# Optimization experiments

Measured on AMD Instinct MI355X. Metric: run time of the kernel, lower is better.

The kernel has to match this reference:

```python
import jax, jax.numpy as jnp
import numpy as np

N_NODES = 100000
N_EDGES = 3200000
N_GRAPHS = 1000
F_IN = 3
H = 64


def setup_inputs() -> dict:
    key = jax.random.key(0)
    ks = jax.random.split(key, 12)
    x = jax.random.normal(ks[0], (N_NODES, F_IN), dtype=jnp.float32)
    edge_index = jax.random.randint(ks[1], (2, N_EDGES), 0, N_NODES, dtype=jnp.int64)
    batch = jnp.sort(jax.random.randint(ks[2], (N_NODES,), 0, N_GRAPHS, dtype=jnp.int64))
    def lin(k, fan_in, fan_out):
        bound = 1.0 / np.sqrt(fan_in)
        return jax.random.uniform(k, (fan_in, fan_out), jnp.float32, -bound, bound)
    return {
        "x": x,
        "edge_index": edge_index,
        "batch": batch,
        "eps1": jax.random.uniform(ks[3], (), jnp.float32),
        "eps2": jax.random.uniform(ks[4], (), jnp.float32),
        "eps3": jax.random.uniform(ks[5], (), jnp.float32),
        "W1": lin(ks[6], F_IN, H), "b1": jnp.zeros((H,), jnp.float32),
        "W2": lin(ks[7], H, H),    "b2": jnp.zeros((H,), jnp.float32),
        "W3": lin(ks[8], H, H),    "b3": jnp.zeros((H,), jnp.float32),
        "Wf1": lin(ks[9], H, 10),  "bf1": jnp.zeros((10,), jnp.float32),
        "Wf2": lin(ks[10], 10, 1), "bf2": jnp.zeros((1,), jnp.float32),
    }


def gin_conv(x, src, dst, eps, W, b):
    # GIN: out = nn((1+eps)*x + sum_{j in N(i)} x_j)
    agg = jax.ops.segment_sum(x[src], dst, num_segments=N_NODES)
    h = (1.0 + eps) * x + agg
    return h @ W + b


def reference(x, edge_index, batch, eps1, eps2, eps3, W1, b1, W2, b2, W3, b3, Wf1, bf1, Wf2, bf2):
    src, dst = edge_index[0], edge_index[1]
    h = jax.nn.relu(gin_conv(x, src, dst, eps1, W1, b1))
    h = jax.nn.relu(gin_conv(h, src, dst, eps2, W2, b2))
    h = jax.nn.relu(gin_conv(h, src, dst, eps3, W3, b3))
    # global mean pool over graphs
    sums = jax.ops.segment_sum(h, batch, num_segments=N_GRAPHS)
    counts = jax.ops.segment_sum(jnp.ones((N_NODES, 1), h.dtype), batch, num_segments=N_GRAPHS)
    pooled = sums / jnp.maximum(counts, 1.0)
    out = jax.nn.relu(pooled @ Wf1 + bf1)
    return out @ Wf2 + bf2
```

## Files before the change

kernel.cpp:

```cpp
#include <hip/hip_runtime.h>

#define N_NODES  100000
#define N_EDGES  3200000
#define N_GRAPHS 1000
#define HDIM     64

#define BUCK_LOG 8
#define BUCK_SZ  256
#define NBUCK    ((N_NODES + BUCK_SZ - 1) / BUCK_SZ)
#define BIN_T    256
#define BIN_E    16
#define BIN_CHUNK (BIN_T * BIN_E)
#define CLUS_CAP 12288

typedef __attribute__((ext_vector_type(8))) short short8;
typedef __attribute__((ext_vector_type(4))) float f32x4;


__device__ inline unsigned short f2bf(float v) {
    unsigned int b; __builtin_memcpy(&b, &v, 4);
    return (unsigned short)((b + 0x7FFFu + ((b >> 16) & 1u)) >> 16);
}
__device__ inline float bf2f(unsigned short u) {
    return __uint_as_float(((unsigned int)u) << 16);
}
__device__ inline void sth(unsigned short* p, float v) { *p = f2bf(v); }
__device__ inline float bflo(unsigned int d) { return __uint_as_float(d << 16); }
__device__ inline float bfhi(unsigned int d) { return __uint_as_float(d & 0xFFFF0000u); }

__device__ inline int clampi(int v, int lo, int hi) {
    return v < lo ? lo : (v > hi ? hi : v);
}


__global__ void k_zero(int* __restrict__ p, int n) {
    int i = blockIdx.x * blockDim.x + threadIdx.x;
    if (i < n) p[i] = 0;
}


__global__ __launch_bounds__(BIN_T) void k_bcount(
        const int* __restrict__ ei, int* __restrict__ btot) {
    __shared__ int hist[NBUCK];
    for (int i = threadIdx.x; i < NBUCK; i += BIN_T) hist[i] = 0;
    __syncthreads();
    int e0 = blockIdx.x * BIN_CHUNK + threadIdx.x;
    #pragma unroll
    for (int k = 0; k < BIN_E; ++k) {
        int e = e0 + k * BIN_T;
        if (e < N_EDGES) {
            int d = clampi(ei[N_EDGES + e], 0, N_NODES - 1);
            atomicAdd(&hist[d >> BUCK_LOG], 1);
        }
    }
    __syncthreads();
    for (int i = threadIdx.x; i < NBUCK; i += BIN_T) {
        int c = hist[i];
        if (c) atomicAdd(&btot[i], c);
    }
}

__global__ void k_bscan(const int* __restrict__ btot, int* __restrict__ bbase,
                        int* __restrict__ gcur, int* __restrict__ off) {
    __shared__ int s[NBUCK + 1];
    int t = threadIdx.x;
    if (t < NBUCK) s[t] = btot[t];
    __syncthreads();
    if (t == 0) {
        int run = 0;
        for (int i = 0; i < NBUCK; ++i) { int x = s[i]; s[i] = run; run += x; }
        s[NBUCK] = run;
    }
    __syncthreads();
    if (t <= NBUCK) bbase[t] = s[t];
    if (t < NBUCK)  gcur[t] = s[t];
    if (t == 0)     off[N_NODES] = s[NBUCK];
}

__global__ __launch_bounds__(BIN_T) void k_bin(
        const int* __restrict__ ei, int* __restrict__ gcur,
        uint2* __restrict__ pairs) {
    __shared__ int hist[NBUCK];
    __shared__ int base[NBUCK];
    for (int i = threadIdx.x; i < NBUCK; i += BIN_T) hist[i] = 0;
    __syncthreads();
    int e0 = blockIdx.x * BIN_CHUNK + threadIdx.x;
    int d[BIN_E], s[BIN_E];
    #pragma unroll
    for (int k = 0; k < BIN_E; ++k) {
        int e = e0 + k * BIN_T;
        bool v = e < N_EDGES;
        d[k] = v ? clampi(ei[N_EDGES + e], 0, N_NODES - 1) : -1;
        s[k] = v ? clampi(ei[e], 0, N_NODES - 1) : 0;
        if (v) atomicAdd(&hist[d[k] >> BUCK_LOG], 1);
    }
    __syncthreads();
    for (int i = threadIdx.x; i < NBUCK; i += BIN_T) {
        int c = hist[i];
        base[i] = c ? atomicAdd(&gcur[i], c) : 0;
        hist[i] = 0;
    }
    __syncthreads();
    #pragma unroll
    for (int k = 0; k < BIN_E; ++k) {
        if (d[k] >= 0) {
            int b = d[k] >> BUCK_LOG;
            int r = atomicAdd(&hist[b], 1);
            uint2 p; p.x = (unsigned)d[k]; p.y = (unsigned)s[k];
            pairs[base[b] + r] = p;
        }
    }
}

__global__ __launch_bounds__(512) void k_cluster(
        const uint2* __restrict__ pairs, const int* __restrict__ bbase,
        int* __restrict__ off, int* __restrict__ adj) {
    __shared__ int ladj[CLUS_CAP];
    __shared__ int lcur[BUCK_SZ];
    __shared__ int lsc[BUCK_SZ];
    int b  = blockIdx.x;
    int lo = b * BUCK_SZ;
    int nn = N_NODES - lo; if (nn > BUCK_SZ) nn = BUCK_SZ;
    int e0 = bbase[b], e1 = bbase[b + 1];
    int cnt = e1 - e0;
    if (threadIdx.x < BUCK_SZ) lcur[threadIdx.x] = 0;
    __syncthreads();
    for (int i = threadIdx.x; i < cnt; i += 512) {
        uint2 p = pairs[e0 + i];
        atomicAdd(&lcur[p.x - lo], 1);
    }
    __syncthreads();
    int v = 0;
    if (threadIdx.x < BUCK_SZ) { v = lcur[threadIdx.x]; lsc[threadIdx.x] = v; }
    __syncthreads();
    #pragma unroll
    for (int d = 1; d < BUCK_SZ; d <<= 1) {
        int add = 0;
        if (threadIdx.x < BUCK_SZ && threadIdx.x >= d) add = lsc[threadIdx.x - d];
        __syncthreads();
        if (threadIdx.x < BUCK_SZ) lsc[threadIdx.x] += add;
        __syncthreads();
    }
    if (threadIdx.x < BUCK_SZ) {
        int exc = lsc[threadIdx.x] - v;
        if (threadIdx.x < nn) off[lo + threadIdx.x] = e0 + exc;
        lcur[threadIdx.x] = exc;
    }
    __syncthreads();
    if (cnt <= CLUS_CAP) {
        for (int i = threadIdx.x; i < cnt; i += 512) {
            uint2 p = pairs[e0 + i];
            int pos = atomicAdd(&lcur[p.x - lo], 1);
            ladj[pos] = (int)p.y;
        }
        __syncthreads();
        for (int i = threadIdx.x; i < cnt; i += 512) adj[e0 + i] = ladj[i];
    } else {
        for (int i = threadIdx.x; i < cnt; i += 512) {
            uint2 p = pairs[e0 + i];
            int pos = atomicAdd(&lcur[p.x - lo], 1);
            adj[e0 + pos] = (int)p.y;
        }
    }
}


__global__ __launch_bounds__(256) void k_layer1(
        const float* __restrict__ x, const int* __restrict__ off,
        const int* __restrict__ adj, const float* __restrict__ epsp,
        const float* __restrict__ W1, const float* __restrict__ b1,
        unsigned short* __restrict__ hout) {
    int wid  = (blockIdx.x * blockDim.x + threadIdx.x) >> 6;
    int lane = threadIdx.x & 63;
    if (wid >= N_NODES) return;
    int o0 = off[wid], o1 = off[wid + 1];
    float a0 = 0.f, a1 = 0.f, a2 = 0.f;
    for (int e = o0 + lane; e < o1; e += 64) {
        int s = adj[e];
        a0 += x[s * 3 + 0];
        a1 += x[s * 3 + 1];
        a2 += x[s * 3 + 2];
    }
    #pragma unroll
    for (int d = 32; d; d >>= 1) {
        a0 += __shfl_xor(a0, d);
        a1 += __shfl_xor(a1, d);
        a2 += __shfl_xor(a2, d);
    }
    float ep = 1.0f + epsp[0];
    float s0 = ep * x[wid * 3 + 0] + a0;
    float s1 = ep * x[wid * 3 + 1] + a1;
    float s2 = ep * x[wid * 3 + 2] + a2;
    float o = b1[lane] + s0 * W1[lane] + s1 * W1[64 + lane] + s2 * W1[128 + lane];
    sth(&hout[(size_t)wid * 64 + lane], fmaxf(o, 0.f));
}


__global__ __launch_bounds__(256) void k_gemm(
        const unsigned short* __restrict__ hin, const float* __restrict__ W,
        unsigned short* __restrict__ Y) {
    int lane = threadIdx.x & 63;
    int r = lane & 15;
    int g = lane >> 4;
    int wave   = blockIdx.x * (blockDim.x >> 6) + (threadIdx.x >> 6);
    int nwaves = gridDim.x * (blockDim.x >> 6);

    short8 bh[2][4], bl[2][4];
    #pragma unroll
    for (int s = 0; s < 2; ++s) {
        #pragma unroll
        for (int t = 0; t < 4; ++t) {
            short8 hv, lv;
            #pragma unroll
            for (int i = 0; i < 8; ++i) {
                int k = s * 32 + g * 8 + i;
                int n = t * 16 + r;
                float w = W[k * 64 + n];
                unsigned short wh = f2bf(w);
                float whf = bf2f(wh);
                hv[i] = (short)wh;
                lv[i] = (short)f2bf(w - whf);
            }
            bh[s][t] = hv; bl[s][t] = lv;
        }
    }

    const int NT = N_NODES / 16;
    for (int mt = wave; mt < NT; mt += nwaves) {
        const unsigned short* arow = hin + (size_t)(mt * 16 + r) * 64;
        short8 a0 = *(const short8*)(arow + g * 8);
        short8 a1 = *(const short8*)(arow + 32 + g * 8);
        #pragma unroll
        for (int t = 0; t < 4; ++t) {
            f32x4 acc = {0.f, 0.f, 0.f, 0.f};
            acc = __builtin_amdgcn_mfma_f32_16x16x32_bf16(a0, bh[0][t], acc, 0, 0, 0);
            acc = __builtin_amdgcn_mfma_f32_16x16x32_bf16(a0, bl[0][t], acc, 0, 0, 0);
            acc = __builtin_amdgcn_mfma_f32_16x16x32_bf16(a1, bh[1][t], acc, 0, 0, 0);
            acc = __builtin_amdgcn_mfma_f32_16x16x32_bf16(a1, bl[1][t], acc, 0, 0, 0);
            #pragma unroll
            for (int j = 0; j < 4; ++j) {
                sth(&Y[(size_t)(mt * 16 + g * 4 + j) * 64 + t * 16 + r], acc[j]);
            }
        }
    }
}


__device__ inline void gather_node(
        const uint2* __restrict__ h2, const int* __restrict__ off,
        const int* __restrict__ adj, int node, int sl, int g4,
        float& a0, float& a1, float& a2, float& a3) {
    int o0 = off[node], o1 = off[node + 1];
    int deg = o1 - o0;
    int nchunk = (deg + 15) >> 4;
    for (int c = 0; c < nchunk; ++c) {
        int pos = o0 + (c << 4) + sl;
        int posc = pos < o1 ? pos : (o1 - 1);
        int idxv = adj[posc];
        int rem = deg - (c << 4);
        #pragma unroll
        for (int half = 0; half < 2; ++half) {
            uint2 dd[8];
            #pragma unroll
            for (int i = 0; i < 8; ++i) {
                int k = half * 8 + i;
                int s = __shfl(idxv, (g4 << 4) + k);
                dd[i] = h2[(size_t)s * 16 + sl];
            }
            #pragma unroll
            for (int i = 0; i < 8; ++i) {
                int k = half * 8 + i;
                int ok = k < rem;
                unsigned int lo = ok ? dd[i].x : 0u;
                unsigned int hc = ok ? dd[i].y : 0u;
                a0 += bflo(lo); a1 += bfhi(lo);
                a2 += bflo(hc); a3 += bfhi(hc);
            }
            if (rem <= 8) break;
        }
    }
}

__global__ __launch_bounds__(1024) void k_gather(
        const unsigned short* __restrict__ Y, const int* __restrict__ off,
        const int* __restrict__ adj, const float* __restrict__ epsp,
        const float* __restrict__ b, unsigned short* __restrict__ hout) {
    int tid  = blockIdx.x * 1024 + threadIdx.x;
    int node = tid >> 4;
    if (node >= N_NODES) return;
    int sl = threadIdx.x & 15;
    int g4 = (threadIdx.x >> 4) & 3;
    const uint2* h2 = (const uint2*)Y;
    float a0 = 0.f, a1 = 0.f, a2 = 0.f, a3 = 0.f;
    gather_node(h2, off, adj, node, sl, g4, a0, a1, a2, a3);
    uint2 ds = h2[(size_t)node * 16 + sl];
    float ep = 1.0f + epsp[0];
    a0 = fmaxf(a0 + ep * bflo(ds.x) + b[4 * sl + 0], 0.f);
    a1 = fmaxf(a1 + ep * bfhi(ds.x) + b[4 * sl + 1], 0.f);
    a2 = fmaxf(a2 + ep * bflo(ds.y) + b[4 * sl + 2], 0.f);
    a3 = fmaxf(a3 + ep * bfhi(ds.y) + b[4 * sl + 3], 0.f);
    uint2 o;
    o.x = (unsigned int)f2bf(a0) | ((unsigned int)f2bf(a1) << 16);
    o.y = (unsigned int)f2bf(a2) | ((unsigned int)f2bf(a3) << 16);
    ((uint2*)hout)[(size_t)node * 16 + sl] = o;
}

__global__ __launch_bounds__(1024) void k_gather_pool(
        const unsigned short* __restrict__ Y, const int* __restrict__ off,
        const int* __restrict__ adj, const float* __restrict__ epsp,
        const float* __restrict__ b, const int* __restrict__ batch,
        float* __restrict__ pooled, int* __restrict__ cnt) {
    __shared__ float sacc[8 * 64];
    __shared__ int   scnt[8];
    for (int i = threadIdx.x; i < 8 * 64; i += 1024) sacc[i] = 0.f;
    if (threadIdx.x < 8) scnt[threadIdx.x] = 0;
    __syncthreads();

    int tid  = blockIdx.x * 1024 + threadIdx.x;
    int node = tid >> 4;
    int sl = threadIdx.x & 15;
    int g4 = (threadIdx.x >> 4) & 3;
    int g0 = clampi(batch[clampi(blockIdx.x << 6, 0, N_NODES - 1)], 0, N_GRAPHS - 1);

    if (node < N_NODES) {
        const uint2* h2 = (const uint2*)Y;
        float a0 = 0.f, a1 = 0.f, a2 = 0.f, a3 = 0.f;
        gather_node(h2, off, adj, node, sl, g4, a0, a1, a2, a3);
        uint2 ds = h2[(size_t)node * 16 + sl];
        float ep = 1.0f + epsp[0];
        a0 = fmaxf(a0 + ep * bflo(ds.x) + b[4 * sl + 0], 0.f);
        a1 = fmaxf(a1 + ep * bfhi(ds.x) + b[4 * sl + 1], 0.f);
        a2 = fmaxf(a2 + ep * bflo(ds.y) + b[4 * sl + 2], 0.f);
        a3 = fmaxf(a3 + ep * bfhi(ds.y) + b[4 * sl + 3], 0.f);
        int g  = clampi(batch[node], 0, N_GRAPHS - 1);
        int og = g - g0;
        if (og >= 0 && og < 8) {
            atomicAdd(&sacc[og * 64 + 4 * sl + 0], a0);
            atomicAdd(&sacc[og * 64 + 4 * sl + 1], a1);
            atomicAdd(&sacc[og * 64 + 4 * sl + 2], a2);
            atomicAdd(&sacc[og * 64 + 4 * sl + 3], a3);
            if (sl == 0) atomicAdd(&scnt[og], 1);
        } else {
            atomicAdd(&pooled[g * 64 + 4 * sl + 0], a0);
            atomicAdd(&pooled[g * 64 + 4 * sl + 1], a1);
            atomicAdd(&pooled[g * 64 + 4 * sl + 2], a2);
            atomicAdd(&pooled[g * 64 + 4 * sl + 3], a3);
            if (sl == 0) atomicAdd(&cnt[g], 1);
        }
    }
    __syncthreads();
    int w = threadIdx.x >> 6;
    int lane = threadIdx.x & 63;
    if (w < 8) {
        int c = scnt[w];
        if (c > 0) {
            atomicAdd(&pooled[(g0 + w) * 64 + lane], sacc[w * 64 + lane]);
            if (lane == 0) atomicAdd(&cnt[g0 + w], c);
        }
    }
}


__global__ __launch_bounds__(256) void k_head(
        const float* __restrict__ pooled, const int* __restrict__ cnt,
        const float* __restrict__ Wf1, const float* __restrict__ bf1,
        const float* __restrict__ Wf2, const float* __restrict__ bf2,
        float* __restrict__ out) {
    int g = blockIdx.x * blockDim.x + threadIdx.x;
    if (g >= N_GRAPHS) return;
    float inv = 1.0f / fmaxf((float)cnt[g], 1.0f);
    float p[64];
    #pragma unroll
    for (int k = 0; k < 64; ++k) p[k] = pooled[g * 64 + k] * inv;
    float o = bf2[0];
    #pragma unroll
    for (int j = 0; j < 10; ++j) {
        float s = bf1[j];
        #pragma unroll
        for (int k = 0; k < 64; ++k) s += p[k] * Wf1[k * 10 + j];
        o += fmaxf(s, 0.f) * Wf2[j];
    }
    out[g] = o;
}


extern "C" void kernel_launch(void* const* d_in, const int* in_sizes, int n_in,
                              void* d_out, int out_size, void* d_ws, size_t ws_size,
                              hipStream_t stream) {
    const float* x     = (const float*)d_in[0];
    const int*   ei    = (const int*)d_in[1];
    const int*   batch = (const int*)d_in[2];
    const float* eps1 = (const float*)d_in[3];
    const float* eps2 = (const float*)d_in[4];
    const float* eps3 = (const float*)d_in[5];
    const float* W1 = (const float*)d_in[6];
    const float* b1 = (const float*)d_in[7];
    const float* W2 = (const float*)d_in[8];
    const float* b2 = (const float*)d_in[9];
    const float* W3 = (const float*)d_in[10];
    const float* b3 = (const float*)d_in[11];
    const float* Wf1 = (const float*)d_in[12];
    const float* bf1 = (const float*)d_in[13];
    const float* Wf2 = (const float*)d_in[14];
    const float* bf2 = (const float*)d_in[15];
    float* out = (float*)d_out;

    const size_t H64 = (size_t)N_NODES * HDIM;

    char* base = (char*)d_ws;
    unsigned short* hA = (unsigned short*)base;
    unsigned short* hB = (unsigned short*)(base + H64 * 2);
    uint2* pairs = (uint2*)base;
    char* q = base + 2 * H64 * 2;
    float* pooled = (float*)q;            q += 64000ull * 4;
    int*   cnt    = (int*)q;              q += 1000ull * 4;
    int*   off    = (int*)q;              q += 100004ull * 4;
    int*   btot   = (int*)q;              q += 512ull * 4;
    int*   bbase  = (int*)q;              q += 512ull * 4;
    int*   gcur   = (int*)q;              q += 512ull * 4;
    int*   adj    = (int*)q;

    const int TB = 256;
    k_zero<<<(65000 + TB - 1) / TB, TB, 0, stream>>>((int*)pooled, 65000);
    k_zero<<<2, TB, 0, stream>>>(btot, NBUCK);

    const int BINB = (N_EDGES + BIN_CHUNK - 1) / BIN_CHUNK;
    k_bcount<<<BINB, BIN_T, 0, stream>>>(ei, btot);
    k_bscan<<<1, 512, 0, stream>>>(btot, bbase, gcur, off);
    k_bin<<<BINB, BIN_T, 0, stream>>>(ei, gcur, pairs);
    k_cluster<<<NBUCK, 512, 0, stream>>>(pairs, bbase, off, adj);

    const int L1_BLOCKS = (int)((H64 + TB - 1) / TB);
    const int GB = (N_NODES * 16 + 1023) / 1024;

    k_layer1<<<L1_BLOCKS, TB, 0, stream>>>(x, off, adj, eps1, W1, b1, hA);
    k_gemm<<<256, 256, 0, stream>>>(hA, W2, hB);
    k_gather<<<GB, 1024, 0, stream>>>(hB, off, adj, eps2, b2, hA);
    k_gemm<<<256, 256, 0, stream>>>(hA, W3, hB);
    k_gather_pool<<<GB, 1024, 0, stream>>>(hB, off, adj, eps3, b3, batch, pooled, cnt);

    k_head<<<(N_GRAPHS + TB - 1) / TB, TB, 0, stream>>>(pooled, cnt, Wf1, bf1, Wf2, bf2, out);
}
```

Before: 283.5 us.

## Vectorize edge binning loads, pack pairs to 32-bit, widen gather to 8 lanes/node

Edge binning kernels now have each thread read 16 contiguous edges through int4 vector loads instead of strided scalar loads. Binned pairs are packed into one 32-bit word holding the in-bucket dst offset and the src index, which halves the pair traffic between binning and clustering. The neighbor gather kernels use 8 lanes per node with 16-byte loads and 8 edges per chunk, in place of 16 lanes with 8-byte loads and 16-edge chunks. The packing assumes src indices fit in 24 bits, and with fewer lanes per node each lane does more serial work per neighbor.

```diff
diff --git a/kernel.cpp b/kernel.cpp
--- a/kernel.cpp
+++ b/kernel.cpp
@@ -15,6 +15,8 @@
 
 typedef __attribute__((ext_vector_type(8))) short short8;
 typedef __attribute__((ext_vector_type(4))) float f32x4;
+typedef __attribute__((ext_vector_type(4))) int   int4v;
+typedef __attribute__((ext_vector_type(4))) unsigned uint4v;
 
 
 __device__ inline unsigned short f2bf(float v) {
@@ -44,13 +46,25 @@
     __shared__ int hist[NBUCK];
     for (int i = threadIdx.x; i < NBUCK; i += BIN_T) hist[i] = 0;
     __syncthreads();
-    int e0 = blockIdx.x * BIN_CHUNK + threadIdx.x;
-    #pragma unroll
-    for (int k = 0; k < BIN_E; ++k) {
-        int e = e0 + k * BIN_T;
-        if (e < N_EDGES) {
-            int d = clampi(ei[N_EDGES + e], 0, N_NODES - 1);
-            atomicAdd(&hist[d >> BUCK_LOG], 1);
+    int e0 = blockIdx.x * BIN_CHUNK + threadIdx.x * BIN_E;
+    if (e0 + BIN_E <= N_EDGES) {
+        const int4v* d4 = (const int4v*)(ei + N_EDGES);
+        #pragma unroll
+        for (int q = 0; q < 4; ++q) {
+            int4v dv = d4[(e0 >> 2) + q];
+            #pragma unroll
+            for (int j = 0; j < 4; ++j) {
+                int d = clampi(dv[j], 0, N_NODES - 1);
+                atomicAdd(&hist[d >> BUCK_LOG], 1);
+            }
+        }
+    } else {
+        for (int k = 0; k < BIN_E; ++k) {
+            int e = e0 + k;
+            if (e < N_EDGES) {
+                int d = clampi(ei[N_EDGES + e], 0, N_NODES - 1);
+                atomicAdd(&hist[d >> BUCK_LOG], 1);
+            }
         }
     }
     __syncthreads();
@@ -79,20 +93,36 @@
 
 __global__ __launch_bounds__(BIN_T) void k_bin(
         const int* __restrict__ ei, int* __restrict__ gcur,
-        uint2* __restrict__ pairs) {
+        unsigned* __restrict__ pairs) {
     __shared__ int hist[NBUCK];
     __shared__ int base[NBUCK];
     for (int i = threadIdx.x; i < NBUCK; i += BIN_T) hist[i] = 0;
     __syncthreads();
-    int e0 = blockIdx.x * BIN_CHUNK + threadIdx.x;
+    int e0 = blockIdx.x * BIN_CHUNK + threadIdx.x * BIN_E;
     int d[BIN_E], s[BIN_E];
-    #pragma unroll
-    for (int k = 0; k < BIN_E; ++k) {
-        int e = e0 + k * BIN_T;
-        bool v = e < N_EDGES;
-        d[k] = v ? clampi(ei[N_EDGES + e], 0, N_NODES - 1) : -1;
-        s[k] = v ? clampi(ei[e], 0, N_NODES - 1) : 0;
-        if (v) atomicAdd(&hist[d[k] >> BUCK_LOG], 1);
+    if (e0 + BIN_E <= N_EDGES) {
+        const int4v* s4 = (const int4v*)ei;
+        const int4v* d4 = (const int4v*)(ei + N_EDGES);
+        #pragma unroll
+        for (int q = 0; q < 4; ++q) {
+            int4v dv = d4[(e0 >> 2) + q];
+            int4v sv = s4[(e0 >> 2) + q];
+            #pragma unroll
+            for (int j = 0; j < 4; ++j) {
+                d[q * 4 + j] = clampi(dv[j], 0, N_NODES - 1);
+                s[q * 4 + j] = clampi(sv[j], 0, N_NODES - 1);
+            }
+        }
+        #pragma unroll
+        for (int k = 0; k < BIN_E; ++k) atomicAdd(&hist[d[k] >> BUCK_LOG], 1);
+    } else {
+        for (int k = 0; k < BIN_E; ++k) {
+            int e = e0 + k;
+            bool v = e < N_EDGES;
+            d[k] = v ? clampi(ei[N_EDGES + e], 0, N_NODES - 1) : -1;
+            s[k] = v ? clampi(ei[e], 0, N_NODES - 1) : 0;
+            if (v) atomicAdd(&hist[d[k] >> BUCK_LOG], 1);
+        }
     }
     __syncthreads();
     for (int i = threadIdx.x; i < NBUCK; i += BIN_T) {
@@ -106,14 +136,13 @@
         if (d[k] >= 0) {
             int b = d[k] >> BUCK_LOG;
             int r = atomicAdd(&hist[b], 1);
-            uint2 p; p.x = (unsigned)d[k]; p.y = (unsigned)s[k];
-            pairs[base[b] + r] = p;
+            pairs[base[b] + r] = ((unsigned)(d[k] & (BUCK_SZ - 1)) << 24) | (unsigned)s[k];
         }
     }
 }
 
 __global__ __launch_bounds__(512) void k_cluster(
-        const uint2* __restrict__ pairs, const int* __restrict__ bbase,
+        const unsigned* __restrict__ pairs, const int* __restrict__ bbase,
         int* __restrict__ off, int* __restrict__ adj) {
     __shared__ int ladj[CLUS_CAP];
     __shared__ int lcur[BUCK_SZ];
@@ -126,8 +155,8 @@
     if (threadIdx.x < BUCK_SZ) lcur[threadIdx.x] = 0;
     __syncthreads();
     for (int i = threadIdx.x; i < cnt; i += 512) {
-        uint2 p = pairs[e0 + i];
-        atomicAdd(&lcur[p.x - lo], 1);
+        unsigned p = pairs[e0 + i];
+        atomicAdd(&lcur[p >> 24], 1);
     }
     __syncthreads();
     int v = 0;
@@ -149,17 +178,17 @@
     __syncthreads();
     if (cnt <= CLUS_CAP) {
         for (int i = threadIdx.x; i < cnt; i += 512) {
-            uint2 p = pairs[e0 + i];
-            int pos = atomicAdd(&lcur[p.x - lo], 1);
-            ladj[pos] = (int)p.y;
+            unsigned p = pairs[e0 + i];
+            int pos = atomicAdd(&lcur[p >> 24], 1);
+            ladj[pos] = (int)(p & 0xFFFFFFu);
         }
         __syncthreads();
         for (int i = threadIdx.x; i < cnt; i += 512) adj[e0 + i] = ladj[i];
     } else {
         for (int i = threadIdx.x; i < cnt; i += 512) {
-            uint2 p = pairs[e0 + i];
-            int pos = atomicAdd(&lcur[p.x - lo], 1);
-            adj[e0 + pos] = (int)p.y;
+            unsigned p = pairs[e0 + i];
+            int pos = atomicAdd(&lcur[p >> 24], 1);
+            adj[e0 + pos] = (int)(p & 0xFFFFFFu);
         }
     }
 }
@@ -246,37 +275,33 @@
 }
 
 
-__device__ inline void gather_node(
-        const uint2* __restrict__ h2, const int* __restrict__ off,
-        const int* __restrict__ adj, int node, int sl, int g4,
-        float& a0, float& a1, float& a2, float& a3) {
+__device__ inline void gather8(
+        const uint4v* __restrict__ h4, const int* __restrict__ off,
+        const int* __restrict__ adj, int node, int sl, int g8, float acc[8]) {
     int o0 = off[node], o1 = off[node + 1];
     int deg = o1 - o0;
-    int nchunk = (deg + 15) >> 4;
-    for (int c = 0; c < nchunk; ++c) {
-        int pos = o0 + (c << 4) + sl;
+    for (int base = 0; base < deg; base += 8) {
+        int pos = o0 + base + sl;
         int posc = pos < o1 ? pos : (o1 - 1);
         int idxv = adj[posc];
-        int rem = deg - (c << 4);
-        #pragma unroll
-        for (int half = 0; half < 2; ++half) {
-            uint2 dd[8];
-            #pragma unroll
-            for (int i = 0; i < 8; ++i) {
-                int k = half * 8 + i;
-                int s = __shfl(idxv, (g4 << 4) + k);
-                dd[i] = h2[(size_t)s * 16 + sl];
-            }
-            #pragma unroll
-            for (int i = 0; i < 8; ++i) {
-                int k = half * 8 + i;
-                int ok = k < rem;
-                unsigned int lo = ok ? dd[i].x : 0u;
-                unsigned int hc = ok ? dd[i].y : 0u;
-                a0 += bflo(lo); a1 += bfhi(lo);
-                a2 += bflo(hc); a3 += bfhi(hc);
-            }
-            if (rem <= 8) break;
+        int rem = deg - base;
+        uint4v dd[8];
+        #pragma unroll
+        for (int k = 0; k < 8; ++k) {
+            int s = __shfl(idxv, (g8 << 3) + k);
+            dd[k] = h4[(size_t)s * 8 + sl];
+        }
+        #pragma unroll
+        for (int k = 0; k < 8; ++k) {
+            bool ok = k < rem;
+            unsigned x0 = ok ? dd[k][0] : 0u;
+            unsigned x1 = ok ? dd[k][1] : 0u;
+            unsigned x2 = ok ? dd[k][2] : 0u;
+            unsigned x3 = ok ? dd[k][3] : 0u;
+            acc[0] += bflo(x0); acc[1] += bfhi(x0);
+            acc[2] += bflo(x1); acc[3] += bfhi(x1);
+            acc[4] += bflo(x2); acc[5] += bfhi(x2);
+            acc[6] += bflo(x3); acc[7] += bfhi(x3);
         }
     }
 }
@@ -286,23 +311,27 @@
         const int* __restrict__ adj, const float* __restrict__ epsp,
         const float* __restrict__ b, unsigned short* __restrict__ hout) {
     int tid  = blockIdx.x * 1024 + threadIdx.x;
-    int node = tid >> 4;
+    int node = tid >> 3;
     if (node >= N_NODES) return;
-    int sl = threadIdx.x & 15;
-    int g4 = (threadIdx.x >> 4) & 3;
-    const uint2* h2 = (const uint2*)Y;
-    float a0 = 0.f, a1 = 0.f, a2 = 0.f, a3 = 0.f;
-    gather_node(h2, off, adj, node, sl, g4, a0, a1, a2, a3);
-    uint2 ds = h2[(size_t)node * 16 + sl];
+    int sl = threadIdx.x & 7;
+    int g8 = (threadIdx.x >> 3) & 7;
+    const uint4v* h4 = (const uint4v*)Y;
+    float acc[8] = {0.f, 0.f, 0.f, 0.f, 0.f, 0.f, 0.f, 0.f};
+    gather8(h4, off, adj, node, sl, g8, acc);
+    uint4v ds = h4[(size_t)node * 8 + sl];
     float ep = 1.0f + epsp[0];
-    a0 = fmaxf(a0 + ep * bflo(ds.x) + b[4 * sl + 0], 0.f);
-    a1 = fmaxf(a1 + ep * bfhi(ds.x) + b[4 * sl + 1], 0.f);
-    a2 = fmaxf(a2 + ep * bflo(ds.y) + b[4 * sl + 2], 0.f);
-    a3 = fmaxf(a3 + ep * bfhi(ds.y) + b[4 * sl + 3], 0.f);
-    uint2 o;
-    o.x = (unsigned int)f2bf(a0) | ((unsigned int)f2bf(a1) << 16);
-    o.y = (unsigned int)f2bf(a2) | ((unsigned int)f2bf(a3) << 16);
-    ((uint2*)hout)[(size_t)node * 16 + sl] = o;
+    acc[0] += ep * bflo(ds[0]); acc[1] += ep * bfhi(ds[0]);
+    acc[2] += ep * bflo(ds[1]); acc[3] += ep * bfhi(ds[1]);
+    acc[4] += ep * bflo(ds[2]); acc[5] += ep * bfhi(ds[2]);
+    acc[6] += ep * bflo(ds[3]); acc[7] += ep * bfhi(ds[3]);
+    uint4v o;
+    #pragma unroll
+    for (int i = 0; i < 4; ++i) {
+        float lo = fmaxf(acc[2 * i]     + b[8 * sl + 2 * i],     0.f);
+        float hi = fmaxf(acc[2 * i + 1] + b[8 * sl + 2 * i + 1], 0.f);
+        o[i] = (unsigned)f2bf(lo) | ((unsigned)f2bf(hi) << 16);
+    }
+    ((uint4v*)hout)[(size_t)node * 8 + sl] = o;
 }
 
 __global__ __launch_bounds__(1024) void k_gather_pool(
@@ -317,34 +346,32 @@
     __syncthreads();
 
     int tid  = blockIdx.x * 1024 + threadIdx.x;
-    int node = tid >> 4;
-    int sl = threadIdx.x & 15;
-    int g4 = (threadIdx.x >> 4) & 3;
-    int g0 = clampi(batch[clampi(blockIdx.x << 6, 0, N_NODES - 1)], 0, N_GRAPHS - 1);
+    int node = tid >> 3;
+    int sl = threadIdx.x & 7;
+    int g8 = (threadIdx.x >> 3) & 7;
+    int g0 = clampi(batch[clampi(blockIdx.x << 7, 0, N_NODES - 1)], 0, N_GRAPHS - 1);
 
     if (node < N_NODES) {
-        const uint2* h2 = (const uint2*)Y;
-        float a0 = 0.f, a1 = 0.f, a2 = 0.f, a3 = 0.f;
-        gather_node(h2, off, adj, node, sl, g4, a0, a1, a2, a3);
-        uint2 ds = h2[(size_t)node * 16 + sl];
+        const uint4v* h4 = (const uint4v*)Y;
+        float acc[8] = {0.f, 0.f, 0.f, 0.f, 0.f, 0.f, 0.f, 0.f};
+        gather8(h4, off, adj, node, sl, g8, acc);
+        uint4v ds = h4[(size_t)node * 8 + sl];
         float ep = 1.0f + epsp[0];
-        a0 = fmaxf(a0 + ep * bflo(ds.x) + b[4 * sl + 0], 0.f);
-        a1 = fmaxf(a1 + ep * bfhi(ds.x) + b[4 * sl + 1], 0.f);
-        a2 = fmaxf(a2 + ep * bflo(ds.y) + b[4 * sl + 2], 0.f);
-        a3 = fmaxf(a3 + ep * bfhi(ds.y) + b[4 * sl + 3], 0.f);
+        acc[0] += ep * bflo(ds[0]); acc[1] += ep * bfhi(ds[0]);
+        acc[2] += ep * bflo(ds[1]); acc[3] += ep * bfhi(ds[1]);
+        acc[4] += ep * bflo(ds[2]); acc[5] += ep * bfhi(ds[2]);
+        acc[6] += ep * bflo(ds[3]); acc[7] += ep * bfhi(ds[3]);
         int g  = clampi(batch[node], 0, N_GRAPHS - 1);
         int og = g - g0;
         if (og >= 0 && og < 8) {
-            atomicAdd(&sacc[og * 64 + 4 * sl + 0], a0);
-            atomicAdd(&sacc[og * 64 + 4 * sl + 1], a1);
-            atomicAdd(&sacc[og * 64 + 4 * sl + 2], a2);
-            atomicAdd(&sacc[og * 64 + 4 * sl + 3], a3);
+            #pragma unroll
+            for (int i = 0; i < 8; ++i)
+                atomicAdd(&sacc[og * 64 + 8 * sl + i], fmaxf(acc[i] + b[8 * sl + i], 0.f));
             if (sl == 0) atomicAdd(&scnt[og], 1);
         } else {
-            atomicAdd(&pooled[g * 64 + 4 * sl + 0], a0);
-            atomicAdd(&pooled[g * 64 + 4 * sl + 1], a1);
-            atomicAdd(&pooled[g * 64 + 4 * sl + 2], a2);
-            atomicAdd(&pooled[g * 64 + 4 * sl + 3], a3);
+            #pragma unroll
+            for (int i = 0; i < 8; ++i)
+                atomicAdd(&pooled[g * 64 + 8 * sl + i], fmaxf(acc[i] + b[8 * sl + i], 0.f));
             if (sl == 0) atomicAdd(&cnt[g], 1);
         }
     }
@@ -410,7 +437,7 @@
     char* base = (char*)d_ws;
     unsigned short* hA = (unsigned short*)base;
     unsigned short* hB = (unsigned short*)(base + H64 * 2);
-    uint2* pairs = (uint2*)base;
+    unsigned* pairs = (unsigned*)base;
     char* q = base + 2 * H64 * 2;
     float* pooled = (float*)q;            q += 64000ull * 4;
     int*   cnt    = (int*)q;              q += 1000ull * 4;
@@ -431,7 +458,7 @@
     k_cluster<<<NBUCK, 512, 0, stream>>>(pairs, bbase, off, adj);
 
     const int L1_BLOCKS = (int)((H64 + TB - 1) / TB);
-    const int GB = (N_NODES * 16 + 1023) / 1024;
+    const int GB = (N_NODES * 8 + 1023) / 1024;
 
     k_layer1<<<L1_BLOCKS, TB, 0, stream>>>(x, off, adj, eps1, W1, b1, hA);
     k_gemm<<<256, 256, 0, stream>>>(hA, W2, hB);
```

After: 305.4 us. 7.7% more time.

## Vectorize edge loads in binning, pack pairs to 32-bit, shrink gather blocks

Applied to the files above, without the earlier changes.

The binning kernels now give each thread a contiguous run of 16 edges and load them with 128-bit vector reads instead of strided scalar reads. Each binned pair is packed into one 32-bit word: the bucket-local destination in the top 8 bits and the source in the low 24. This halves the pairs traffic written by k_bin and read twice by k_cluster. The gather kernels drop from 1024 to 512 threads per block, which should help scheduling and occupancy; the packing relies on node ids fitting in 24 bits.

```diff
diff --git a/kernel.cpp b/kernel.cpp
--- a/kernel.cpp
+++ b/kernel.cpp
@@ -15,6 +15,7 @@
 
 typedef __attribute__((ext_vector_type(8))) short short8;
 typedef __attribute__((ext_vector_type(4))) float f32x4;
+typedef __attribute__((ext_vector_type(4))) int   int4v;
 
 
 __device__ inline unsigned short f2bf(float v) {
@@ -44,13 +45,25 @@
     __shared__ int hist[NBUCK];
     for (int i = threadIdx.x; i < NBUCK; i += BIN_T) hist[i] = 0;
     __syncthreads();
-    int e0 = blockIdx.x * BIN_CHUNK + threadIdx.x;
-    #pragma unroll
-    for (int k = 0; k < BIN_E; ++k) {
-        int e = e0 + k * BIN_T;
-        if (e < N_EDGES) {
-            int d = clampi(ei[N_EDGES + e], 0, N_NODES - 1);
-            atomicAdd(&hist[d >> BUCK_LOG], 1);
+    int e0 = blockIdx.x * BIN_CHUNK + threadIdx.x * BIN_E;
+    if (e0 + BIN_E <= N_EDGES) {
+        const int4v* d4 = (const int4v*)(ei + N_EDGES);
+        #pragma unroll
+        for (int q = 0; q < 4; ++q) {
+            int4v dv = d4[(e0 >> 2) + q];
+            #pragma unroll
+            for (int j = 0; j < 4; ++j) {
+                int d = clampi(dv[j], 0, N_NODES - 1);
+                atomicAdd(&hist[d >> BUCK_LOG], 1);
+            }
+        }
+    } else {
+        for (int k = 0; k < BIN_E; ++k) {
+            int e = e0 + k;
+            if (e < N_EDGES) {
+                int d = clampi(ei[N_EDGES + e], 0, N_NODES - 1);
+                atomicAdd(&hist[d >> BUCK_LOG], 1);
+            }
         }
     }
     __syncthreads();
@@ -79,20 +92,36 @@
 
 __global__ __launch_bounds__(BIN_T) void k_bin(
         const int* __restrict__ ei, int* __restrict__ gcur,
-        uint2* __restrict__ pairs) {
+        unsigned* __restrict__ pairs) {
     __shared__ int hist[NBUCK];
     __shared__ int base[NBUCK];
     for (int i = threadIdx.x; i < NBUCK; i += BIN_T) hist[i] = 0;
     __syncthreads();
-    int e0 = blockIdx.x * BIN_CHUNK + threadIdx.x;
+    int e0 = blockIdx.x * BIN_CHUNK + threadIdx.x * BIN_E;
     int d[BIN_E], s[BIN_E];
-    #pragma unroll
-    for (int k = 0; k < BIN_E; ++k) {
-        int e = e0 + k * BIN_T;
-        bool v = e < N_EDGES;
-        d[k] = v ? clampi(ei[N_EDGES + e], 0, N_NODES - 1) : -1;
-        s[k] = v ? clampi(ei[e], 0, N_NODES - 1) : 0;
-        if (v) atomicAdd(&hist[d[k] >> BUCK_LOG], 1);
+    if (e0 + BIN_E <= N_EDGES) {
+        const int4v* s4 = (const int4v*)ei;
+        const int4v* d4 = (const int4v*)(ei + N_EDGES);
+        #pragma unroll
+        for (int q = 0; q < 4; ++q) {
+            int4v dv = d4[(e0 >> 2) + q];
+            int4v sv = s4[(e0 >> 2) + q];
+            #pragma unroll
+            for (int j = 0; j < 4; ++j) {
+                d[q * 4 + j] = clampi(dv[j], 0, N_NODES - 1);
+                s[q * 4 + j] = clampi(sv[j], 0, N_NODES - 1);
+            }
+        }
+        #pragma unroll
+        for (int k = 0; k < BIN_E; ++k) atomicAdd(&hist[d[k] >> BUCK_LOG], 1);
+    } else {
+        for (int k = 0; k < BIN_E; ++k) {
+            int e = e0 + k;
+            bool v = e < N_EDGES;
+            d[k] = v ? clampi(ei[N_EDGES + e], 0, N_NODES - 1) : -1;
+            s[k] = v ? clampi(ei[e], 0, N_NODES - 1) : 0;
+            if (v) atomicAdd(&hist[d[k] >> BUCK_LOG], 1);
+        }
     }
     __syncthreads();
     for (int i = threadIdx.x; i < NBUCK; i += BIN_T) {
@@ -106,14 +135,13 @@
         if (d[k] >= 0) {
             int b = d[k] >> BUCK_LOG;
             int r = atomicAdd(&hist[b], 1);
-            uint2 p; p.x = (unsigned)d[k]; p.y = (unsigned)s[k];
-            pairs[base[b] + r] = p;
+            pairs[base[b] + r] = ((unsigned)(d[k] & (BUCK_SZ - 1)) << 24) | (unsigned)s[k];
         }
     }
 }
 
 __global__ __launch_bounds__(512) void k_cluster(
-        const uint2* __restrict__ pairs, const int* __restrict__ bbase,
+        const unsigned* __restrict__ pairs, const int* __restrict__ bbase,
         int* __restrict__ off, int* __restrict__ adj) {
     __shared__ int ladj[CLUS_CAP];
     __shared__ int lcur[BUCK_SZ];
@@ -126,8 +154,8 @@
     if (threadIdx.x < BUCK_SZ) lcur[threadIdx.x] = 0;
     __syncthreads();
     for (int i = threadIdx.x; i < cnt; i += 512) {
-        uint2 p = pairs[e0 + i];
-        atomicAdd(&lcur[p.x - lo], 1);
+        unsigned p = pairs[e0 + i];
+        atomicAdd(&lcur[p >> 24], 1);
     }
     __syncthreads();
     int v = 0;
@@ -149,17 +177,17 @@
     __syncthreads();
     if (cnt <= CLUS_CAP) {
         for (int i = threadIdx.x; i < cnt; i += 512) {
-            uint2 p = pairs[e0 + i];
-            int pos = atomicAdd(&lcur[p.x - lo], 1);
-            ladj[pos] = (int)p.y;
+            unsigned p = pairs[e0 + i];
+            int pos = atomicAdd(&lcur[p >> 24], 1);
+            ladj[pos] = (int)(p & 0xFFFFFFu);
         }
         __syncthreads();
         for (int i = threadIdx.x; i < cnt; i += 512) adj[e0 + i] = ladj[i];
     } else {
         for (int i = threadIdx.x; i < cnt; i += 512) {
-            uint2 p = pairs[e0 + i];
-            int pos = atomicAdd(&lcur[p.x - lo], 1);
-            adj[e0 + pos] = (int)p.y;
+            unsigned p = pairs[e0 + i];
+            int pos = atomicAdd(&lcur[p >> 24], 1);
+            adj[e0 + pos] = (int)(p & 0xFFFFFFu);
         }
     }
 }
@@ -281,11 +309,11 @@
     }
 }
 
-__global__ __launch_bounds__(1024) void k_gather(
+__global__ __launch_bounds__(512) void k_gather(
         const unsigned short* __restrict__ Y, const int* __restrict__ off,
         const int* __restrict__ adj, const float* __restrict__ epsp,
         const float* __restrict__ b, unsigned short* __restrict__ hout) {
-    int tid  = blockIdx.x * 1024 + threadIdx.x;
+    int tid  = blockIdx.x * 512 + threadIdx.x;
     int node = tid >> 4;
     if (node >= N_NODES) return;
     int sl = threadIdx.x & 15;
@@ -305,22 +333,22 @@
     ((uint2*)hout)[(size_t)node * 16 + sl] = o;
 }
 
-__global__ __launch_bounds__(1024) void k_gather_pool(
+__global__ __launch_bounds__(512) void k_gather_pool(
         const unsigned short* __restrict__ Y, const int* __restrict__ off,
         const int* __restrict__ adj, const float* __restrict__ epsp,
         const float* __restrict__ b, const int* __restrict__ batch,
         float* __restrict__ pooled, int* __restrict__ cnt) {
     __shared__ float sacc[8 * 64];
     __shared__ int   scnt[8];
-    for (int i = threadIdx.x; i < 8 * 64; i += 1024) sacc[i] = 0.f;
+    for (int i = threadIdx.x; i < 8 * 64; i += 512) sacc[i] = 0.f;
     if (threadIdx.x < 8) scnt[threadIdx.x] = 0;
     __syncthreads();
 
-    int tid  = blockIdx.x * 1024 + threadIdx.x;
+    int tid  = blockIdx.x * 512 + threadIdx.x;
     int node = tid >> 4;
     int sl = threadIdx.x & 15;
     int g4 = (threadIdx.x >> 4) & 3;
-    int g0 = clampi(batch[clampi(blockIdx.x << 6, 0, N_NODES - 1)], 0, N_GRAPHS - 1);
+    int g0 = clampi(batch[clampi(blockIdx.x * 32, 0, N_NODES - 1)], 0, N_GRAPHS - 1);
 
     if (node < N_NODES) {
         const uint2* h2 = (const uint2*)Y;
@@ -410,7 +438,7 @@
     char* base = (char*)d_ws;
     unsigned short* hA = (unsigned short*)base;
     unsigned short* hB = (unsigned short*)(base + H64 * 2);
-    uint2* pairs = (uint2*)base;
+    unsigned* pairs = (unsigned*)base;
     char* q = base + 2 * H64 * 2;
     float* pooled = (float*)q;            q += 64000ull * 4;
     int*   cnt    = (int*)q;              q += 1000ull * 4;
@@ -431,13 +459,13 @@
     k_cluster<<<NBUCK, 512, 0, stream>>>(pairs, bbase, off, adj);
 
     const int L1_BLOCKS = (int)((H64 + TB - 1) / TB);
-    const int GB = (N_NODES * 16 + 1023) / 1024;
+    const int GB = (N_NODES * 16 + 511) / 512;
 
     k_layer1<<<L1_BLOCKS, TB, 0, stream>>>(x, off, adj, eps1, W1, b1, hA);
     k_gemm<<<256, 256, 0, stream>>>(hA, W2, hB);
-    k_gather<<<GB, 1024, 0, stream>>>(hB, off, adj, eps2, b2, hA);
+    k_gather<<<GB, 512, 0, stream>>>(hB, off, adj, eps2, b2, hA);
     k_gemm<<<256, 256, 0, stream>>>(hA, W3, hB);
-    k_gather_pool<<<GB, 1024, 0, stream>>>(hB, off, adj, eps3, b3, batch, pooled, cnt);
+    k_gather_pool<<<GB, 512, 0, stream>>>(hB, off, adj, eps3, b3, batch, pooled, cnt);
 
     k_head<<<(N_GRAPHS + TB - 1) / TB, TB, 0, stream>>>(pooled, cnt, Wf1, bf1, Wf2, bf2, out);
 }
```

Measured after the change: 266.5 us. -6.0%, faster.
